# Kernel optimization log

Measured on AMD Instinct MI355X. Metric: run time of the kernel, lower is better.

Reference implementation:

```python
import jax, jax.numpy as jnp
import numpy as np

ROUTING_ITERS = 3
EPS = 1e-07


def setup_inputs() -> dict:
    key = jax.random.key(0)
    k1, k2 = jax.random.split(key)
    B, IN_CAPS, OUT_CAPS, POSE = 128, 2048, 32, 4
    votes = jax.random.normal(k1, (B, IN_CAPS, OUT_CAPS, POSE), dtype=jnp.float32)
    activations_in = jax.random.uniform(k2, (B, IN_CAPS), dtype=jnp.float32)
    return {"votes": votes, "activations_in": activations_in}


def _safe_norm(s, axis=-1):
    # NOTE: original safe_norm always keeps dims (reduce_sum keepdims=True, then sqrt)
    return jnp.sqrt(jnp.sum(jnp.square(s), axis=axis, keepdims=True) + EPS)


def _squash(s):
    s_norm = _safe_norm(s, axis=-1)                 # [..., 1]
    scale = jnp.square(s_norm) / (1.0 + jnp.square(s_norm))
    return scale * (s / s_norm)


def reference(votes, activations_in):
    # votes: [B, in_caps, out_caps, pose]
    B, in_caps, out_caps, _ = votes.shape
    b_ij = jnp.zeros((B, in_caps, out_caps), dtype=jnp.float32)
    v_j = None
    for _ in range(ROUTING_ITERS):
        c_ij = jax.nn.softmax(b_ij, axis=2)                       # [B, I, O]
        s_j = jnp.einsum('bio,biop->bop', c_ij, votes)            # [B, O, P]
        v_j = _squash(s_j)                                        # [B, O, P]
        v_stop = jax.lax.stop_gradient(v_j)
        agreement = jnp.einsum('biop,bop->bio', votes, v_stop)    # [B, I, O]
        b_ij = b_ij + agreement
    poses_out = v_j                                               # [B, O, P]
    activations_out = _safe_norm(poses_out, axis=-1)              # [B, O, 1] (keepdims bug preserved)
    return poses_out, activations_out
```

## Files before the change

### kernel.cpp

```cpp
#include <hip/hip_runtime.h>


#define BATCH 128
#define IC 2048
#define OC 32
#define POSE 4
#define REPS 1e-7f
#define CHUNKS 16
#define CHUNK_I (IC / CHUNKS)
#define BLOCK_T 256
#define GROUPS (BLOCK_T / 32)
#define ILP 4
#define STEPS (CHUNK_I / (GROUPS * ILP))

#define PART_IDX(t, b, c, o) ((((size_t)(t) * BATCH + (b)) * CHUNKS + (c)) * OC + (o))

__device__ __forceinline__ float dot4(const float4 a, const float4 b) {
    return a.x*b.x + a.y*b.y + a.z*b.z + a.w*b.w;
}

__device__ __forceinline__ float4 squash4(const float4 s) {
    const float n2 = s.x*s.x + s.y*s.y + s.z*s.z + s.w*s.w + REPS;
    const float f = n2 / (1.f + n2) * rsqrtf(n2);
    return make_float4(f*s.x, f*s.y, f*s.z, f*s.w);
}

__device__ __forceinline__ float4 reduce_squash(
    const float4* __restrict__ partials, int t, int b, int o, float scale)
{
    float4 acc = make_float4(0.f, 0.f, 0.f, 0.f);
    #pragma unroll
    for (int c = 0; c < CHUNKS; ++c) {
        const float4 p = partials[PART_IDX(t, b, c, o)];
        acc.x += p.x; acc.y += p.y; acc.z += p.z; acc.w += p.w;
    }
    acc.x *= scale; acc.y *= scale; acc.z *= scale; acc.w *= scale;
    return squash4(acc);
}

template <int T>
__global__ __launch_bounds__(BLOCK_T) void routing_accum(
    const float4* __restrict__ votes,
    float4* __restrict__ partials)
{
    const int blk   = blockIdx.x;
    const int b     = blk >> 4;
    const int chunk = blk & (CHUNKS - 1);
    const int o     = threadIdx.x & 31;
    const int g     = threadIdx.x >> 5;

    __shared__ float4 lds_s[GROUPS * 32];
    __shared__ float4 vh0_s[32];
    __shared__ float4 vh1_s[32];

    if (T >= 1 && threadIdx.x < 32) {
        vh0_s[o] = reduce_squash(partials, 0, b, o, 1.f / 32.f);
        if (T >= 2) vh1_s[o] = reduce_squash(partials, 1, b, o, 1.f);
    }
    if (T >= 1) __syncthreads();
    float4 vh0 = (T >= 1) ? vh0_s[o] : make_float4(0.f, 0.f, 0.f, 0.f);
    float4 vh1 = (T >= 2) ? vh1_s[o] : make_float4(0.f, 0.f, 0.f, 0.f);

    float4 s_acc = make_float4(0.f, 0.f, 0.f, 0.f);
    const float4* vb = votes + (size_t)b * IC * OC;
    const int i0 = chunk * CHUNK_I;

    #pragma unroll
    for (int step = 0; step < STEPS; ++step) {
        const int ia = i0 + step * (GROUPS * ILP) + g;
        float4 v0 = vb[(size_t)(ia + 0 * GROUPS) * OC + o];
        float4 v1 = vb[(size_t)(ia + 1 * GROUPS) * OC + o];
        float4 v2 = vb[(size_t)(ia + 2 * GROUPS) * OC + o];
        float4 v3 = vb[(size_t)(ia + 3 * GROUPS) * OC + o];

        if (T == 0) {
            s_acc.x += (v0.x + v1.x) + (v2.x + v3.x);
            s_acc.y += (v0.y + v1.y) + (v2.y + v3.y);
            s_acc.z += (v0.z + v1.z) + (v2.z + v3.z);
            s_acc.w += (v0.w + v1.w) + (v2.w + v3.w);
        } else {
            float l0 = dot4(v0, vh0);
            float l1 = dot4(v1, vh0);
            float l2 = dot4(v2, vh0);
            float l3 = dot4(v3, vh0);
            if (T >= 2) {
                l0 += dot4(v0, vh1); l1 += dot4(v1, vh1);
                l2 += dot4(v2, vh1); l3 += dot4(v3, vh1);
            }
            float e0 = __expf(l0), e1 = __expf(l1), e2 = __expf(l2), e3 = __expf(l3);
            float t0 = e0, t1 = e1, t2 = e2, t3 = e3;
            #pragma unroll
            for (int d = 16; d >= 1; d >>= 1) {
                t0 += __shfl_xor(t0, d);
                t1 += __shfl_xor(t1, d);
                t2 += __shfl_xor(t2, d);
                t3 += __shfl_xor(t3, d);
            }
            const float c0 = e0 * __builtin_amdgcn_rcpf(t0);
            const float c1 = e1 * __builtin_amdgcn_rcpf(t1);
            const float c2 = e2 * __builtin_amdgcn_rcpf(t2);
            const float c3 = e3 * __builtin_amdgcn_rcpf(t3);

            s_acc.x += c0*v0.x + c1*v1.x + c2*v2.x + c3*v3.x;
            s_acc.y += c0*v0.y + c1*v1.y + c2*v2.y + c3*v3.y;
            s_acc.z += c0*v0.z + c1*v1.z + c2*v2.z + c3*v3.z;
            s_acc.w += c0*v0.w + c1*v1.w + c2*v2.w + c3*v3.w;
        }
    }

    __syncthreads();
    lds_s[g * 32 + o] = s_acc;
    __syncthreads();

    if (threadIdx.x < 32) {
        float4 tot = lds_s[o];
        #pragma unroll
        for (int gg = 1; gg < GROUPS; ++gg) {
            const float4 x = lds_s[gg * 32 + o];
            tot.x += x.x; tot.y += x.y; tot.z += x.z; tot.w += x.w;
        }
        partials[PART_IDX(T, b, chunk, o)] = tot;
    }
}

__global__ void routing_finalize(
    const float4* __restrict__ partials,
    float* __restrict__ out)
{
    const int idx = blockIdx.x * blockDim.x + threadIdx.x;
    if (idx >= BATCH * OC) return;
    const int b = idx >> 5, o = idx & 31;
    const float4 v = reduce_squash(partials, 2, b, o, 1.f);
    ((float4*)out)[idx] = v;
    const float a = sqrtf(v.x*v.x + v.y*v.y + v.z*v.z + v.w*v.w + REPS);
    out[BATCH * OC * POSE + idx] = a;
}

extern "C" void kernel_launch(void* const* d_in, const int* in_sizes, int n_in,
                              void* d_out, int out_size, void* d_ws, size_t ws_size,
                              hipStream_t stream) {
    const float4* votes = (const float4*)d_in[0];
    float4* partials = (float4*)d_ws;

    routing_accum<0><<<BATCH * CHUNKS, BLOCK_T, 0, stream>>>(votes, partials);
    routing_accum<1><<<BATCH * CHUNKS, BLOCK_T, 0, stream>>>(votes, partials);
    routing_accum<2><<<BATCH * CHUNKS, BLOCK_T, 0, stream>>>(votes, partials);
    routing_finalize<<<(BATCH * OC + 255) / 256, 256, 0, stream>>>(
        partials, (float*)d_out);
}
```

Before: 237.5 us.

## Cache votes as fp16 copy in first pass and read it in later routing passes

The first routing pass now also writes a half-precision copy of the votes into workspace, and the two later passes read that compact copy instead of the fp32 input. This cuts memory traffic for the later passes and may let the smaller copy stay in the on-chip cache. The two squashed pose vectors are also summed once so each logit needs a single dot product. The cost is an extra write in pass one, reduced precision of the votes in later iterations, and reliance on the workspace being large enough.

```diff
diff --git a/kernel.cpp b/kernel.cpp
--- a/kernel.cpp
+++ b/kernel.cpp
@@ -1,4 +1,5 @@
 #include <hip/hip_runtime.h>
+#include <hip/hip_fp16.h>
 
 
 #define BATCH 128
@@ -15,6 +16,20 @@
 
 #define PART_IDX(t, b, c, o) ((((size_t)(t) * BATCH + (b)) * CHUNKS + (c)) * OC + (o))
 
+struct alignas(8) half4v { __half2 xy, zw; };
+
+__device__ __forceinline__ half4v f2h(const float4 v) {
+    half4v h;
+    h.xy = __float22half2_rn(make_float2(v.x, v.y));
+    h.zw = __float22half2_rn(make_float2(v.z, v.w));
+    return h;
+}
+__device__ __forceinline__ float4 h2f(const half4v h) {
+    const float2 a = __half22float2(h.xy);
+    const float2 b = __half22float2(h.zw);
+    return make_float4(a.x, a.y, b.x, b.y);
+}
+
 __device__ __forceinline__ float dot4(const float4 a, const float4 b) {
     return a.x*b.x + a.y*b.y + a.z*b.z + a.w*b.w;
 }
@@ -38,80 +53,12 @@
     return squash4(acc);
 }
 
-template <int T>
-__global__ __launch_bounds__(BLOCK_T) void routing_accum(
-    const float4* __restrict__ votes,
-    float4* __restrict__ partials)
-{
-    const int blk   = blockIdx.x;
-    const int b     = blk >> 4;
-    const int chunk = blk & (CHUNKS - 1);
-    const int o     = threadIdx.x & 31;
-    const int g     = threadIdx.x >> 5;
-
-    __shared__ float4 lds_s[GROUPS * 32];
-    __shared__ float4 vh0_s[32];
-    __shared__ float4 vh1_s[32];
-
-    if (T >= 1 && threadIdx.x < 32) {
-        vh0_s[o] = reduce_squash(partials, 0, b, o, 1.f / 32.f);
-        if (T >= 2) vh1_s[o] = reduce_squash(partials, 1, b, o, 1.f);
-    }
-    if (T >= 1) __syncthreads();
-    float4 vh0 = (T >= 1) ? vh0_s[o] : make_float4(0.f, 0.f, 0.f, 0.f);
-    float4 vh1 = (T >= 2) ? vh1_s[o] : make_float4(0.f, 0.f, 0.f, 0.f);
-
-    float4 s_acc = make_float4(0.f, 0.f, 0.f, 0.f);
-    const float4* vb = votes + (size_t)b * IC * OC;
-    const int i0 = chunk * CHUNK_I;
-
-    #pragma unroll
-    for (int step = 0; step < STEPS; ++step) {
-        const int ia = i0 + step * (GROUPS * ILP) + g;
-        float4 v0 = vb[(size_t)(ia + 0 * GROUPS) * OC + o];
-        float4 v1 = vb[(size_t)(ia + 1 * GROUPS) * OC + o];
-        float4 v2 = vb[(size_t)(ia + 2 * GROUPS) * OC + o];
-        float4 v3 = vb[(size_t)(ia + 3 * GROUPS) * OC + o];
-
-        if (T == 0) {
-            s_acc.x += (v0.x + v1.x) + (v2.x + v3.x);
-            s_acc.y += (v0.y + v1.y) + (v2.y + v3.y);
-            s_acc.z += (v0.z + v1.z) + (v2.z + v3.z);
-            s_acc.w += (v0.w + v1.w) + (v2.w + v3.w);
-        } else {
-            float l0 = dot4(v0, vh0);
-            float l1 = dot4(v1, vh0);
-            float l2 = dot4(v2, vh0);
-            float l3 = dot4(v3, vh0);
-            if (T >= 2) {
-                l0 += dot4(v0, vh1); l1 += dot4(v1, vh1);
-                l2 += dot4(v2, vh1); l3 += dot4(v3, vh1);
-            }
-            float e0 = __expf(l0), e1 = __expf(l1), e2 = __expf(l2), e3 = __expf(l3);
-            float t0 = e0, t1 = e1, t2 = e2, t3 = e3;
-            #pragma unroll
-            for (int d = 16; d >= 1; d >>= 1) {
-                t0 += __shfl_xor(t0, d);
-                t1 += __shfl_xor(t1, d);
-                t2 += __shfl_xor(t2, d);
-                t3 += __shfl_xor(t3, d);
-            }
-            const float c0 = e0 * __builtin_amdgcn_rcpf(t0);
-            const float c1 = e1 * __builtin_amdgcn_rcpf(t1);
-            const float c2 = e2 * __builtin_amdgcn_rcpf(t2);
-            const float c3 = e3 * __builtin_amdgcn_rcpf(t3);
-
-            s_acc.x += c0*v0.x + c1*v1.x + c2*v2.x + c3*v3.x;
-            s_acc.y += c0*v0.y + c1*v1.y + c2*v2.y + c3*v3.y;
-            s_acc.z += c0*v0.z + c1*v1.z + c2*v2.z + c3*v3.z;
-            s_acc.w += c0*v0.w + c1*v1.w + c2*v2.w + c3*v3.w;
-        }
-    }
-
-    __syncthreads();
+__device__ __forceinline__ void block_reduce_store(
+    float4 s_acc, float4* lds_s, float4* __restrict__ partials,
+    int t, int b, int chunk, int g, int o)
+{
     lds_s[g * 32 + o] = s_acc;
     __syncthreads();
-
     if (threadIdx.x < 32) {
         float4 tot = lds_s[o];
         #pragma unroll
@@ -119,8 +66,118 @@
             const float4 x = lds_s[gg * 32 + o];
             tot.x += x.x; tot.y += x.y; tot.z += x.z; tot.w += x.w;
         }
-        partials[PART_IDX(T, b, chunk, o)] = tot;
-    }
+        partials[PART_IDX(t, b, chunk, o)] = tot;
+    }
+}
+
+__global__ __launch_bounds__(BLOCK_T) void routing_pass0(
+    const float4* __restrict__ votes,
+    half4v* __restrict__ v16,
+    float4* __restrict__ partials)
+{
+    const int blk   = blockIdx.x;
+    const int b     = blk >> 4;
+    const int chunk = blk & (CHUNKS - 1);
+    const int o     = threadIdx.x & 31;
+    const int g     = threadIdx.x >> 5;
+
+    __shared__ float4 lds_s[GROUPS * 32];
+
+    float4 s_acc = make_float4(0.f, 0.f, 0.f, 0.f);
+    const float4* vb = votes + (size_t)b * IC * OC;
+    half4v* cb = v16 + (size_t)b * IC * OC;
+    const int i0 = chunk * CHUNK_I;
+
+    #pragma unroll
+    for (int step = 0; step < STEPS; ++step) {
+        const int ia = i0 + step * (GROUPS * ILP) + g;
+        const size_t e0 = (size_t)(ia + 0 * GROUPS) * OC + o;
+        const size_t e1 = (size_t)(ia + 1 * GROUPS) * OC + o;
+        const size_t e2 = (size_t)(ia + 2 * GROUPS) * OC + o;
+        const size_t e3 = (size_t)(ia + 3 * GROUPS) * OC + o;
+        const float4 v0 = vb[e0];
+        const float4 v1 = vb[e1];
+        const float4 v2 = vb[e2];
+        const float4 v3 = vb[e3];
+
+        s_acc.x += (v0.x + v1.x) + (v2.x + v3.x);
+        s_acc.y += (v0.y + v1.y) + (v2.y + v3.y);
+        s_acc.z += (v0.z + v1.z) + (v2.z + v3.z);
+        s_acc.w += (v0.w + v1.w) + (v2.w + v3.w);
+
+        cb[e0] = f2h(v0);
+        cb[e1] = f2h(v1);
+        cb[e2] = f2h(v2);
+        cb[e3] = f2h(v3);
+    }
+
+    block_reduce_store(s_acc, lds_s, partials, 0, b, chunk, g, o);
+}
+
+template <int T>
+__global__ __launch_bounds__(BLOCK_T) void routing_accum(
+    const half4v* __restrict__ v16,
+    float4* __restrict__ partials)
+{
+    const int blk   = blockIdx.x;
+    const int b     = blk >> 4;
+    const int chunk = blk & (CHUNKS - 1);
+    const int o     = threadIdx.x & 31;
+    const int g     = threadIdx.x >> 5;
+
+    __shared__ float4 lds_s[GROUPS * 32];
+    __shared__ float4 vh0_s[32];
+    __shared__ float4 vh1_s[32];
+
+    if (threadIdx.x < 32) {
+        vh0_s[o] = reduce_squash(partials, 0, b, o, 1.f / 32.f);
+        if (T >= 2) vh1_s[o] = reduce_squash(partials, 1, b, o, 1.f);
+    }
+    __syncthreads();
+    float4 vh = vh0_s[o];
+    if (T >= 2) {
+        const float4 h1 = vh1_s[o];
+        vh.x += h1.x; vh.y += h1.y; vh.z += h1.z; vh.w += h1.w;
+    }
+
+    float4 s_acc = make_float4(0.f, 0.f, 0.f, 0.f);
+    const half4v* cb = v16 + (size_t)b * IC * OC;
+    const int i0 = chunk * CHUNK_I;
+
+    #pragma unroll
+    for (int step = 0; step < STEPS; ++step) {
+        const int ia = i0 + step * (GROUPS * ILP) + g;
+        const float4 v0 = h2f(cb[(size_t)(ia + 0 * GROUPS) * OC + o]);
+        const float4 v1 = h2f(cb[(size_t)(ia + 1 * GROUPS) * OC + o]);
+        const float4 v2 = h2f(cb[(size_t)(ia + 2 * GROUPS) * OC + o]);
+        const float4 v3 = h2f(cb[(size_t)(ia + 3 * GROUPS) * OC + o]);
+
+        const float l0 = dot4(v0, vh);
+        const float l1 = dot4(v1, vh);
+        const float l2 = dot4(v2, vh);
+        const float l3 = dot4(v3, vh);
+        float e0 = __expf(l0), e1 = __expf(l1), e2 = __expf(l2), e3 = __expf(l3);
+        float t0 = e0, t1 = e1, t2 = e2, t3 = e3;
+        #pragma unroll
+        for (int d = 16; d >= 1; d >>= 1) {
+            t0 += __shfl_xor(t0, d);
+            t1 += __shfl_xor(t1, d);
+            t2 += __shfl_xor(t2, d);
+            t3 += __shfl_xor(t3, d);
+        }
+        const float c0 = e0 * __builtin_amdgcn_rcpf(t0);
+        const float c1 = e1 * __builtin_amdgcn_rcpf(t1);
+        const float c2 = e2 * __builtin_amdgcn_rcpf(t2);
+        const float c3 = e3 * __builtin_amdgcn_rcpf(t3);
+
+        s_acc.x += c0*v0.x + c1*v1.x + c2*v2.x + c3*v3.x;
+        s_acc.y += c0*v0.y + c1*v1.y + c2*v2.y + c3*v3.y;
+        s_acc.z += c0*v0.z + c1*v1.z + c2*v2.z + c3*v3.z;
+        s_acc.w += c0*v0.w + c1*v1.w + c2*v2.w + c3*v3.w;
+    }
+
+    __syncthreads();
+    block_reduce_store(s_acc, lds_s, partials, T, b, chunk, g, o);
 }
 
 __global__ void routing_finalize(
@@ -140,11 +197,13 @@
                               void* d_out, int out_size, void* d_ws, size_t ws_size,
                               hipStream_t stream) {
     const float4* votes = (const float4*)d_in[0];
+
     float4* partials = (float4*)d_ws;
-
-    routing_accum<0><<<BATCH * CHUNKS, BLOCK_T, 0, stream>>>(votes, partials);
-    routing_accum<1><<<BATCH * CHUNKS, BLOCK_T, 0, stream>>>(votes, partials);
-    routing_accum<2><<<BATCH * CHUNKS, BLOCK_T, 0, stream>>>(votes, partials);
+    half4v* v16 = (half4v*)((char*)d_ws + (size_t)3 * BATCH * CHUNKS * OC * sizeof(float4));
+
+    routing_pass0<<<BATCH * CHUNKS, BLOCK_T, 0, stream>>>(votes, v16, partials);
+    routing_accum<1><<<BATCH * CHUNKS, BLOCK_T, 0, stream>>>(v16, partials);
+    routing_accum<2><<<BATCH * CHUNKS, BLOCK_T, 0, stream>>>(v16, partials);
     routing_finalize<<<(BATCH * OC + 255) / 256, 256, 0, stream>>>(
         partials, (float*)d_out);
 }
```

New measurement: 230.4 us. 1.03x faster.
